# Kernel optimization log

Hardware: AMD Instinct MI355X
Metric: run time of the kernel (lower is better)

## Reference

```python
import jax, jax.numpy as jnp
import numpy as np

# Neuron hyperparameters (mid-range of the optuna search space)
THRESHOLD = 1.0
CURRENT_DECAY = 0.3
VOLTAGE_DECAY = 0.8
TAU_GRAD = 0.5
SCALE_GRAD = 1.0

B, N_IN, H, N_OUT, T = 64, 2048, 1024, 2, 128
SPIKE_RATE = 0.1  # input spike density


@jax.custom_vjp
def spike_fn(v):
    # Heaviside spike with SLAYER exponential surrogate gradient
    return (v >= 0.0).astype(v.dtype)

def _spike_fwd(v):
    return spike_fn(v), v

def _spike_bwd(v, g):
    return (g * SCALE_GRAD * jnp.exp(-jnp.abs(v) / TAU_GRAD),)

spike_fn.defvjp(_spike_fwd, _spike_bwd)


def cuba_dense(spike, W):
    """One SLAYER CUBA Dense block: dense synapse + leaky IF neuron over time.
    spike: [B, N_in, T], W: [N_out, N_in] -> [B, N_out, T] output spikes."""
    z = jnp.einsum('oi,bit->tbo', W, spike)  # synaptic current input, [T, B, O]
    O = W.shape[0]
    zeros = jnp.zeros((spike.shape[0], O), spike.dtype)

    def step(carry, z_t):
        cur, vol = carry
        cur = cur * (1.0 - CURRENT_DECAY) + z_t          # current dynamics
        vol = vol * (1.0 - VOLTAGE_DECAY) + cur          # voltage dynamics
        s = spike_fn(vol - THRESHOLD)                    # threshold spike
        vol = vol * (1.0 - s)                            # reset to zero on spike
        return (cur, vol), s

    _, s = jax.lax.scan(step, (zeros, zeros), z)
    return jnp.transpose(s, (1, 2, 0))  # [B, O, T]


def setup_inputs() -> dict:
    key = jax.random.key(0)
    k0, k1, k2, k3 = jax.random.split(key, 4)
    spike = (jax.random.uniform(k0, (B, N_IN, T)) < SPIKE_RATE).astype(jnp.float32)
    W1 = jax.random.normal(k1, (H, N_IN), jnp.float32) / np.sqrt(N_IN).astype(np.float32)
    W2 = jax.random.normal(k2, (H, H), jnp.float32) / np.sqrt(H).astype(np.float32)
    W3 = jax.random.normal(k3, (N_OUT, H), jnp.float32) / np.sqrt(H).astype(np.float32)
    return {"spike": spike, "W1": W1, "W2": W2, "W3": W3}


def reference(spike, W1, W2, W3):
    s = cuba_dense(spike, W1)
    s = cuba_dense(s, W2)
    s = cuba_dense(s, W3)
    return s  # [B, 2, T]
```

## Files before the change

### kernel.cpp

```cpp
#include <hip/hip_runtime.h>


typedef unsigned short ushort_t;
typedef unsigned int uint_t;
typedef __bf16 bf16x8 __attribute__((ext_vector_type(8)));
typedef float f32x4 __attribute__((ext_vector_type(4)));

#define O_TOT 1024

__device__ __forceinline__ void glds16(const ushort_t* g, ushort_t* l) {
  __builtin_amdgcn_global_load_lds(
      (const __attribute__((address_space(1))) uint_t*)g,
      (__attribute__((address_space(3))) uint_t*)l, 16, 0, 0);
}

__device__ __forceinline__ ushort_t f32_to_bf16_rne(float f) {
  uint_t u = __float_as_uint(f);
  u += 0x7FFFu + ((u >> 16) & 1u);
  return (ushort_t)(u >> 16);
}

__global__ __launch_bounds__(256) void prep(const float* __restrict__ W1,
                                            const float* __restrict__ W2,
                                            const float* __restrict__ spike,
                                            ushort_t* __restrict__ h1,
                                            ushort_t* __restrict__ l1,
                                            ushort_t* __restrict__ h2,
                                            ushort_t* __restrict__ l2,
                                            ushort_t* __restrict__ A1) {
  const int tid = threadIdx.x;
  if (blockIdx.x < 12288) {
    int idx = blockIdx.x * 256 + tid;
    const int N1 = 1024 * 2048;
    if (idx < N1) {
      float w = W1[idx];
      ushort_t h = f32_to_bf16_rne(w);
      h1[idx] = h;
      l1[idx] = f32_to_bf16_rne(w - __uint_as_float(((uint_t)h) << 16));
    } else {
      int k = idx - N1;
      float w = W2[k];
      ushort_t h = f32_to_bf16_rne(w);
      h2[k] = h;
      l2[k] = f32_to_bf16_rne(w - __uint_as_float(((uint_t)h) << 16));
    }
    return;
  }
  __shared__ ushort_t lds[128 * 130];
  const int bid = blockIdx.x - 12288;
  const int b = bid >> 4;
  const int i0 = (bid & 15) * 128;
#pragma unroll
  for (int it = 0; it < 16; ++it) {
    int p = it * 256 + tid;
    int i = p >> 5, tg = (p & 31) * 4;
    float4 v = *(const float4*)(spike + ((size_t)b * 2048 + i0 + i) * 128 + tg);
    lds[i * 130 + tg + 0] = (v.x != 0.0f) ? 0x3F80u : 0u;
    lds[i * 130 + tg + 1] = (v.y != 0.0f) ? 0x3F80u : 0u;
    lds[i * 130 + tg + 2] = (v.z != 0.0f) ? 0x3F80u : 0u;
    lds[i * 130 + tg + 3] = (v.w != 0.0f) ? 0x3F80u : 0u;
  }
  __syncthreads();
#pragma unroll
  for (int it = 0; it < 16; ++it) {
    int p = it * 256 + tid;
    int t = p >> 5, j = p & 31;
    uint_t u0 = (uint_t)lds[(4 * j + 0) * 130 + t] | ((uint_t)lds[(4 * j + 1) * 130 + t] << 16);
    uint_t u1 = (uint_t)lds[(4 * j + 2) * 130 + t] | ((uint_t)lds[(4 * j + 3) * 130 + t] << 16);
    uint2* dst = (uint2*)(A1 + (size_t)(b * 128 + t) * 2048 + i0);
    dst[j] = make_uint2(u0, u1);
  }
}

__global__ __launch_bounds__(256, 4)
void gemm_scan(const ushort_t* __restrict__ A, const ushort_t* __restrict__ Bhi,
               const ushort_t* __restrict__ Blo, ushort_t* __restrict__ S,
               int K) {
  __shared__ float smemf[128 * 65];
  ushort_t* As = (ushort_t*)smemf;
  ushort_t* Bh = As + 8192;
  ushort_t* Bl = Bh + 4096;
  float* Zt = smemf;

  const int tid = threadIdx.x;
  const int wave = tid >> 6, lane = tid & 63;
  const int b = blockIdx.y;
  const int m0 = b * 128;
  const int o0 = blockIdx.x * 64;
  const int qm = wave >> 1, qn = wave & 1;
  const int fr = lane & 15, q = lane >> 4;

  f32x4 acc[4][2];
#pragma unroll
  for (int i = 0; i < 4; ++i)
#pragma unroll
    for (int j = 0; j < 2; ++j) acc[i][j] = (f32x4){0.f, 0.f, 0.f, 0.f};

  size_t gA[4];
  ushort_t* lA[4];
#pragma unroll
  for (int r = 0; r < 4; ++r) {
    int s = wave * 256 + r * 64 + lane;
    int row = s >> 3;
    int u = (s & 7) ^ (row & 7);
    gA[r] = (size_t)(m0 + row) * K + u * 8;
    lA[r] = As + (size_t)(wave * 256 + r * 64) * 8;
  }
  size_t gB[2];
  ushort_t *lBh[2], *lBl[2];
#pragma unroll
  for (int r = 0; r < 2; ++r) {
    int s = wave * 128 + r * 64 + lane;
    int row = s >> 3;
    int u = (s & 7) ^ (row & 7);
    gB[r] = (size_t)(o0 + row) * K + u * 8;
    lBh[r] = Bh + (size_t)(wave * 128 + r * 64) * 8;
    lBl[r] = Bl + (size_t)(wave * 128 + r * 64) * 8;
  }

  int aoff[4][2], boff[2][2];
#pragma unroll
  for (int i = 0; i < 4; ++i)
#pragma unroll
    for (int kk = 0; kk < 2; ++kk) {
      int row = qm * 64 + i * 16 + fr;
      int u = (kk * 4 + q) ^ (row & 7);
      aoff[i][kk] = row * 64 + u * 8;
    }
#pragma unroll
  for (int j = 0; j < 2; ++j)
#pragma unroll
    for (int kk = 0; kk < 2; ++kk) {
      int row = qn * 32 + j * 16 + fr;
      int u = (kk * 4 + q) ^ (row & 7);
      boff[j][kk] = row * 64 + u * 8;
    }

  for (int kc = 0; kc < K; kc += 64) {
#pragma unroll
    for (int r = 0; r < 4; ++r) glds16(A + gA[r] + kc, lA[r]);
#pragma unroll
    for (int r = 0; r < 2; ++r) {
      glds16(Bhi + gB[r] + kc, lBh[r]);
      glds16(Blo + gB[r] + kc, lBl[r]);
    }
    __syncthreads();

#pragma unroll
    for (int kk = 0; kk < 2; ++kk) {
      bf16x8 af[4], bh[2], bl[2];
#pragma unroll
      for (int i = 0; i < 4; ++i) af[i] = *(const bf16x8*)(As + aoff[i][kk]);
#pragma unroll
      for (int j = 0; j < 2; ++j) {
        bh[j] = *(const bf16x8*)(Bh + boff[j][kk]);
        bl[j] = *(const bf16x8*)(Bl + boff[j][kk]);
      }
#pragma unroll
      for (int i = 0; i < 4; ++i)
#pragma unroll
        for (int j = 0; j < 2; ++j) {
          acc[i][j] = __builtin_amdgcn_mfma_f32_16x16x32_bf16(af[i], bh[j], acc[i][j], 0, 0, 0);
          acc[i][j] = __builtin_amdgcn_mfma_f32_16x16x32_bf16(af[i], bl[j], acc[i][j], 0, 0, 0);
        }
    }
    __syncthreads();
  }

#pragma unroll
  for (int i = 0; i < 4; ++i)
#pragma unroll
    for (int j = 0; j < 2; ++j)
#pragma unroll
      for (int rr = 0; rr < 4; ++rr)
        Zt[(qm * 64 + i * 16 + q * 4 + rr) * 65 + qn * 32 + j * 16 + fr] = acc[i][j][rr];
  __syncthreads();

  if (tid < 64) {
#pragma clang fp contract(off)
    float cur = 0.0f, vol = 0.0f;
    const int o = o0 + tid;
    for (int t = 0; t < 128; ++t) {
      float z = Zt[t * 65 + tid];
      cur = cur * 0.7f;
      cur = cur + z;
      vol = vol * 0.2f;
      vol = vol + cur;
      float v = vol - 1.0f;
      float s = (v >= 0.0f) ? 1.0f : 0.0f;
      vol = vol * (1.0f - s);
      S[(size_t)(m0 + t) * O_TOT + o] = (v >= 0.0f) ? 0x3F80u : 0u;
    }
  }
}

__global__ __launch_bounds__(256) void gemm3_scan(const ushort_t* __restrict__ X,
                                                  const float* __restrict__ W3,
                                                  float* __restrict__ out) {
  __shared__ float w3s[2048];
  __shared__ float z3[256];
  __shared__ float sp[256];
  const int tid = threadIdx.x;
  const int b = blockIdx.x;
  for (int i = tid; i < 2048; i += 256) w3s[i] = W3[i];
  __syncthreads();
  const int wave = tid >> 6, lane = tid & 63;
  for (int tt = 0; tt < 32; ++tt) {
    int t = wave * 32 + tt;
    const uint_t* row = (const uint_t*)(X + (size_t)(b * 128 + t) * 1024) + lane * 8;
    float s0 = 0.0f, s1 = 0.0f;
#pragma unroll
    for (int jw = 0; jw < 8; ++jw) {
      uint_t u = row[jw];
      float x0 = __uint_as_float(u << 16);
      float x1 = __uint_as_float(u & 0xFFFF0000u);
      int i0 = lane * 16 + jw * 2;
      s0 = fmaf(x0, w3s[i0], s0);
      s1 = fmaf(x0, w3s[1024 + i0], s1);
      s0 = fmaf(x1, w3s[i0 + 1], s0);
      s1 = fmaf(x1, w3s[1024 + i0 + 1], s1);
    }
#pragma unroll
    for (int off = 32; off > 0; off >>= 1) {
      s0 += __shfl_down(s0, off);
      s1 += __shfl_down(s1, off);
    }
    if (lane == 0) {
      z3[t * 2] = s0;
      z3[t * 2 + 1] = s1;
    }
  }
  __syncthreads();
  if (tid < 2) {
#pragma clang fp contract(off)
    float cur = 0.0f, vol = 0.0f;
    for (int t = 0; t < 128; ++t) {
      float z = z3[t * 2 + tid];
      cur = cur * 0.7f;
      cur = cur + z;
      vol = vol * 0.2f;
      vol = vol + cur;
      float v = vol - 1.0f;
      float s = (v >= 0.0f) ? 1.0f : 0.0f;
      vol = vol * (1.0f - s);
      sp[tid * 128 + t] = s;
    }
  }
  __syncthreads();
  out[b * 256 + tid] = sp[tid];
}

extern "C" void kernel_launch(void* const* d_in, const int* in_sizes, int n_in,
                              void* d_out, int out_size, void* d_ws, size_t ws_size,
                              hipStream_t stream) {
  const float* spike = (const float*)d_in[0];
  const float* W1 = (const float*)d_in[1];
  const float* W2 = (const float*)d_in[2];
  const float* W3 = (const float*)d_in[3];
  float* out = (float*)d_out;

  char* ws = (char*)d_ws;
  ushort_t* A1 = (ushort_t*)ws;
  ushort_t* S2 = (ushort_t*)(ws + (size_t)32 * 1024 * 1024);
  ushort_t* S3 = (ushort_t*)(ws + (size_t)48 * 1024 * 1024);
  ushort_t* W1hi = (ushort_t*)(ws + (size_t)64 * 1024 * 1024);
  ushort_t* W1lo = (ushort_t*)(ws + (size_t)68 * 1024 * 1024);
  ushort_t* W2hi = (ushort_t*)(ws + (size_t)72 * 1024 * 1024);
  ushort_t* W2lo = (ushort_t*)(ws + (size_t)74 * 1024 * 1024);

  prep<<<13312, 256, 0, stream>>>(W1, W2, spike, W1hi, W1lo, W2hi, W2lo, A1);
  gemm_scan<<<dim3(16, 64), 256, 0, stream>>>(A1, W1hi, W1lo, S2, 2048);
  gemm_scan<<<dim3(16, 64), 256, 0, stream>>>(S2, W2hi, W2lo, S3, 1024);
  gemm3_scan<<<64, 256, 0, stream>>>(S3, W3, out);
}
```

Baseline: 237.7 us.

## Pre-swizzle weight hi/lo into MFMA fragment order and load B directly to registers

The prep kernel now writes the bf16 hi/lo weight splits in a permuted layout that matches the per-lane MFMA B-fragment order for each 64-wide output tile and 64-deep K chunk. The GEMM then loads B fragments straight from global memory into registers with contiguous 16-byte loads, skipping LDS staging for B. This removes LDS traffic and footprint for B, but the B loads are now plain global loads issued every K step and are not shared across the two waves that use the same fragments.

```diff
diff --git a/kernel.cpp b/kernel.cpp
--- a/kernel.cpp
+++ b/kernel.cpp
@@ -30,20 +30,28 @@
                                             ushort_t* __restrict__ A1) {
   const int tid = threadIdx.x;
   if (blockIdx.x < 12288) {
-    int idx = blockIdx.x * 256 + tid;
-    const int N1 = 1024 * 2048;
-    if (idx < N1) {
-      float w = W1[idx];
-      ushort_t h = f32_to_bf16_rne(w);
-      h1[idx] = h;
-      l1[idx] = f32_to_bf16_rne(w - __uint_as_float(((uint_t)h) << 16));
+    const float* W;
+    ushort_t *hp, *lp;
+    int idx, K;
+    if (blockIdx.x < 8192) {
+      idx = blockIdx.x * 256 + tid;
+      W = W1; hp = h1; lp = l1; K = 2048;
     } else {
-      int k = idx - N1;
-      float w = W2[k];
-      ushort_t h = f32_to_bf16_rne(w);
-      h2[k] = h;
-      l2[k] = f32_to_bf16_rne(w - __uint_as_float(((uint_t)h) << 16));
-    }
+      idx = (blockIdx.x - 8192) * 256 + tid;
+      W = W2; hp = h2; lp = l2; K = 1024;
+    }
+    int e = idx & 7, fr = (idx >> 3) & 15, q = (idx >> 7) & 3;
+    int kk = (idx >> 9) & 1, j = (idx >> 10) & 1, qn = (idx >> 11) & 1;
+    int rest = idx >> 12;
+    int kcm = (K == 2048) ? 31 : 15;
+    int kcs = (K == 2048) ? 5 : 4;
+    int kc = rest & kcm, o_blk = rest >> kcs;
+    int o = o_blk * 64 + qn * 32 + j * 16 + fr;
+    int k = kc * 64 + kk * 32 + q * 8 + e;
+    float w = W[(size_t)o * K + k];
+    ushort_t h = f32_to_bf16_rne(w);
+    hp[idx] = h;
+    lp[idx] = f32_to_bf16_rne(w - __uint_as_float(((uint_t)h) << 16));
     return;
   }
   __shared__ ushort_t lds[128 * 130];
@@ -73,13 +81,11 @@
 }
 
 __global__ __launch_bounds__(256, 4)
-void gemm_scan(const ushort_t* __restrict__ A, const ushort_t* __restrict__ Bhi,
-               const ushort_t* __restrict__ Blo, ushort_t* __restrict__ S,
+void gemm_scan(const ushort_t* __restrict__ A, const ushort_t* __restrict__ Bhp,
+               const ushort_t* __restrict__ Blp, ushort_t* __restrict__ S,
                int K) {
   __shared__ float smemf[128 * 65];
   ushort_t* As = (ushort_t*)smemf;
-  ushort_t* Bh = As + 8192;
-  ushort_t* Bl = Bh + 4096;
   float* Zt = smemf;
 
   const int tid = threadIdx.x;
@@ -106,62 +112,46 @@
     gA[r] = (size_t)(m0 + row) * K + u * 8;
     lA[r] = As + (size_t)(wave * 256 + r * 64) * 8;
   }
-  size_t gB[2];
-  ushort_t *lBh[2], *lBl[2];
-#pragma unroll
-  for (int r = 0; r < 2; ++r) {
-    int s = wave * 128 + r * 64 + lane;
-    int row = s >> 3;
-    int u = (s & 7) ^ (row & 7);
-    gB[r] = (size_t)(o0 + row) * K + u * 8;
-    lBh[r] = Bh + (size_t)(wave * 128 + r * 64) * 8;
-    lBl[r] = Bl + (size_t)(wave * 128 + r * 64) * 8;
-  }
-
-  int aoff[4][2], boff[2][2];
+
+  int aoff[4][2];
 #pragma unroll
   for (int i = 0; i < 4; ++i)
 #pragma unroll
     for (int kk = 0; kk < 2; ++kk) {
       int row = qm * 64 + i * 16 + fr;
-      int u = (kk * 4 + q) ^ (row & 7);
-      aoff[i][kk] = row * 64 + u * 8;
-    }
-#pragma unroll
-  for (int j = 0; j < 2; ++j)
+      aoff[i][kk] = row * 64 + (((kk * 4 + q) ^ (row & 7))) * 8;
+    }
+
+  const size_t pbase = ((size_t)blockIdx.x * (K >> 6)) * 4096 + qn * 2048 + lane * 8;
+  const ushort_t* pBh = Bhp + pbase;
+  const ushort_t* pBl = Blp + pbase;
+
+  for (int kc = 0; kc < K; kc += 64) {
+    bf16x8 bh[2][2], bl[2][2];
+    const ushort_t* ph = pBh + (size_t)(kc >> 6) * 4096;
+    const ushort_t* pl = pBl + (size_t)(kc >> 6) * 4096;
+#pragma unroll
+    for (int j = 0; j < 2; ++j)
+#pragma unroll
+      for (int kk = 0; kk < 2; ++kk) {
+        bh[j][kk] = *(const bf16x8*)(ph + j * 1024 + kk * 512);
+        bl[j][kk] = *(const bf16x8*)(pl + j * 1024 + kk * 512);
+      }
+#pragma unroll
+    for (int r = 0; r < 4; ++r) glds16(A + gA[r] + kc, lA[r]);
+    __syncthreads();
+
 #pragma unroll
     for (int kk = 0; kk < 2; ++kk) {
-      int row = qn * 32 + j * 16 + fr;
-      int u = (kk * 4 + q) ^ (row & 7);
-      boff[j][kk] = row * 64 + u * 8;
-    }
-
-  for (int kc = 0; kc < K; kc += 64) {
-#pragma unroll
-    for (int r = 0; r < 4; ++r) glds16(A + gA[r] + kc, lA[r]);
-#pragma unroll
-    for (int r = 0; r < 2; ++r) {
-      glds16(Bhi + gB[r] + kc, lBh[r]);
-      glds16(Blo + gB[r] + kc, lBl[r]);
-    }
-    __syncthreads();
-
-#pragma unroll
-    for (int kk = 0; kk < 2; ++kk) {
-      bf16x8 af[4], bh[2], bl[2];
+      bf16x8 af[4];
 #pragma unroll
       for (int i = 0; i < 4; ++i) af[i] = *(const bf16x8*)(As + aoff[i][kk]);
 #pragma unroll
-      for (int j = 0; j < 2; ++j) {
-        bh[j] = *(const bf16x8*)(Bh + boff[j][kk]);
-        bl[j] = *(const bf16x8*)(Bl + boff[j][kk]);
-      }
-#pragma unroll
       for (int i = 0; i < 4; ++i)
 #pragma unroll
         for (int j = 0; j < 2; ++j) {
-          acc[i][j] = __builtin_amdgcn_mfma_f32_16x16x32_bf16(af[i], bh[j], acc[i][j], 0, 0, 0);
-          acc[i][j] = __builtin_amdgcn_mfma_f32_16x16x32_bf16(af[i], bl[j], acc[i][j], 0, 0, 0);
+          acc[i][j] = __builtin_amdgcn_mfma_f32_16x16x32_bf16(af[i], bh[j][kk], acc[i][j], 0, 0, 0);
+          acc[i][j] = __builtin_amdgcn_mfma_f32_16x16x32_bf16(af[i], bl[j][kk], acc[i][j], 0, 0, 0);
         }
     }
     __syncthreads();
```

After: 251.5 us. +5.8%, slower.
